# Kernel tuning notes

Hardware: AMD Instinct MI355X
Metric: run time of the kernel (lower is better)

Reference implementation:

```python
import jax, jax.numpy as jnp
import numpy as np

N, E, D = 100000, 1600000, 128      # nodes, edges, in_channels = MLP out_dim
L = 3                               # num GIN layers
OC = D + L * D                      # concat width = 512
CH, CHID = 4, 256                   # num ChannelMLPs, their hidden dim


def setup_inputs() -> dict:
    key = jax.random.key(0)
    ks = jax.random.split(key, 10)
    s = lambda fan_in: 1.0 / np.sqrt(fan_in)
    x = jax.random.normal(ks[0], (N, D), dtype=jnp.float32)
    edge_index = jax.random.randint(ks[1], (2, E), 0, N, dtype=jnp.int32)
    # conv MLPs: per layer 3 linear layers (in->hid, hid->hid, hid->out), all 128x128
    convW = jax.random.normal(ks[2], (L, 3, D, D), dtype=jnp.float32) * s(D)
    convB = jnp.zeros((L, 3, D), dtype=jnp.float32)
    # channel MLPs: 512 -> 256 -> 256 -> 1, ReLU after every layer (output_activation='relu')
    chanW1 = jax.random.normal(ks[3], (CH, OC, CHID), dtype=jnp.float32) * s(OC)
    chanB1 = jnp.zeros((CH, CHID), dtype=jnp.float32)
    chanW2 = jax.random.normal(ks[4], (CH, CHID, CHID), dtype=jnp.float32) * s(CHID)
    chanB2 = jnp.zeros((CH, CHID), dtype=jnp.float32)
    chanW3 = jax.random.normal(ks[5], (CH, CHID, 1), dtype=jnp.float32) * s(CHID)
    chanB3 = jnp.zeros((CH, 1), dtype=jnp.float32)
    return {"x": x, "edge_index": edge_index, "convW": convW, "convB": convB,
            "chanW1": chanW1, "chanB1": chanB1, "chanW2": chanW2, "chanB2": chanB2,
            "chanW3": chanW3, "chanB3": chanB3}


def reference(x, edge_index, convW, convB, chanW1, chanB1, chanW2, chanB2, chanW3, chanB3):
    src, dst = edge_index[0], edge_index[1]
    n = x.shape[0]
    feats = [x]                      # skip_first_features=False -> keep input
    h = x
    for l in range(L):
        # GINConv, eps=0: mlp((1+eps)*h + sum_{j in N(i)} h_j)
        agg = jax.ops.segment_sum(h[src], dst, num_segments=n)  # scatter-add at targets
        h = h + agg
        for k in range(3):           # MLP: Lin+ReLU x3 (2 hidden + relu output activation)
            h = jax.nn.relu(h @ convW[l, k] + convB[l, k])
        feats.append(h)
    xcat = jnp.concatenate(feats, axis=1)                       # [N, 512]
    # channel MLPs vectorized over the channel axis c
    h1 = jax.nn.relu(jnp.einsum('nd,cdh->cnh', xcat, chanW1) + chanB1[:, None, :])
    h2 = jax.nn.relu(jnp.einsum('cnh,chk->cnk', h1, chanW2) + chanB2[:, None, :])
    h3 = jax.nn.relu(jnp.einsum('cnh,cho->cno', h2, chanW3) + chanB3[:, None, :])
    return jnp.transpose(h3[..., 0])                            # [N, num_ChannelMLPs]
```

## Files before the change

kernel.cpp:

```cpp
#include <hip/hip_runtime.h>
#include <hip/hip_bf16.h>

#define D 128
#define NLAYER 3
#define NCH 4

typedef __attribute__((ext_vector_type(8))) short short8;
typedef __attribute__((ext_vector_type(4))) float f32x4;

__device__ __forceinline__ ushort f2bf(float f) {
    unsigned int u = __builtin_bit_cast(unsigned int, f);
    u += 0x7fffu + ((u >> 16) & 1u);
    return (ushort)(u >> 16);
}
__device__ __forceinline__ float bflo(unsigned int u) {
    return __builtin_bit_cast(float, u << 16);
}
__device__ __forceinline__ float bfhi(unsigned int u) {
    return __builtin_bit_cast(float, u & 0xffff0000u);
}

#define FILL_CHUNK 4096
__global__ __launch_bounds__(256) void hist_part_kernel(
    const int* __restrict__ dst, int* __restrict__ deg,
    int E, int nPer, int N)
{
    int cls = blockIdx.x & 7;
    int base = (blockIdx.x >> 3) * FILL_CHUNK;
    int lo = cls * nPer;
    int hi = lo + nPer; if (hi > N) hi = N;
    int end = base + FILL_CHUNK; if (end > E) end = E;
    for (int e = base + threadIdx.x; e < end; e += 256) {
        int d = dst[e];
        if (d >= lo && d < hi) atomicAdd(&deg[d], 1);
    }
}

__global__ __launch_bounds__(256) void blocksum_kernel(
    const int* __restrict__ deg, int* __restrict__ bsum, int n)
{
    int i = blockIdx.x * 256 + threadIdx.x;
    int v = (i < n) ? deg[i] : 0;
#pragma unroll
    for (int o = 1; o < 64; o <<= 1) v += __shfl_xor(v, o);
    __shared__ int s[4];
    if ((threadIdx.x & 63) == 0) s[threadIdx.x >> 6] = v;
    __syncthreads();
    if (threadIdx.x == 0) bsum[blockIdx.x] = s[0] + s[1] + s[2] + s[3];
}

__global__ __launch_bounds__(512) void scanblk_kernel(
    const int* __restrict__ bsum, int* __restrict__ boff, int nb,
    int* __restrict__ offs, int n, int E)
{
    __shared__ int sh[512];
    int t = threadIdx.x;
    sh[t] = (t < nb) ? bsum[t] : 0;
    __syncthreads();
    for (int d = 1; d < 512; d <<= 1) {
        int v = (t >= d) ? sh[t - d] : 0;
        __syncthreads();
        sh[t] += v;
        __syncthreads();
    }
    if (t < nb) boff[t] = (t == 0) ? 0 : sh[t - 1];
    if (t == 0) offs[n] = E;
}

__global__ __launch_bounds__(256) void blockscan_kernel(
    const int* __restrict__ deg, const int* __restrict__ boff,
    int* __restrict__ offs, int* __restrict__ cursor, int n)
{
    __shared__ int sh[256];
    int t = threadIdx.x;
    int i = blockIdx.x * 256 + t;
    int v = (i < n) ? deg[i] : 0;
    sh[t] = v;
    __syncthreads();
    for (int d = 1; d < 256; d <<= 1) {
        int u = (t >= d) ? sh[t - d] : 0;
        __syncthreads();
        sh[t] += u;
        __syncthreads();
    }
    if (i < n) {
        int ex = boff[blockIdx.x] + sh[t] - v;
        offs[i] = ex; cursor[i] = ex;
    }
}

__global__ __launch_bounds__(256) void fill_part_kernel(
    const int* __restrict__ src, const int* __restrict__ dst,
    int* __restrict__ cursor, int* __restrict__ csr,
    int E, int nPer, int N)
{
    int cls = blockIdx.x & 7;
    int base = (blockIdx.x >> 3) * FILL_CHUNK;
    int lo = cls * nPer;
    int hi = lo + nPer; if (hi > N) hi = N;
    int end = base + FILL_CHUNK; if (end > E) end = E;
    for (int e = base + threadIdx.x; e < end; e += 256) {
        int d = dst[e];
        int s = src[e];
        if (d >= lo && d < hi) {
            int p = atomicAdd(&cursor[d], 1);
            csr[p] = s;
        }
    }
}

__global__ __launch_bounds__(256) void cvtx_kernel(
    const float* __restrict__ x, ushort* __restrict__ xb, int total8)
{
    int i = blockIdx.x * 256 + threadIdx.x;
    if (i >= total8) return;
    const float* gp = x + (size_t)i * 8;
    float4 v0 = *(const float4*)gp;
    float4 v1 = *(const float4*)(gp + 4);
    short8 pk;
    pk[0] = (short)f2bf(v0.x); pk[1] = (short)f2bf(v0.y);
    pk[2] = (short)f2bf(v0.z); pk[3] = (short)f2bf(v0.w);
    pk[4] = (short)f2bf(v1.x); pk[5] = (short)f2bf(v1.y);
    pk[6] = (short)f2bf(v1.z); pk[7] = (short)f2bf(v1.w);
    *(short8*)(xb + (size_t)i * 8) = pk;
}

__global__ void cvtW_kernel(const float* __restrict__ W, ushort* __restrict__ Wt,
                            int K, int Ncols) {
    __shared__ float tile[32][33];
    int c = blockIdx.z;
    int k0 = blockIdx.x * 32, n0 = blockIdx.y * 32;
    const float* Wc = W + (size_t)c * K * Ncols;
    ushort* Wtc = Wt + (size_t)c * K * Ncols;
    int tx = threadIdx.x & 31, ty = threadIdx.x >> 5;
#pragma unroll
    for (int i = 0; i < 4; ++i) {
        int k = k0 + ty + i * 8;
        tile[ty + i * 8][tx] = Wc[(size_t)k * Ncols + n0 + tx];
    }
    __syncthreads();
#pragma unroll
    for (int i = 0; i < 4; ++i) {
        int n = n0 + ty + i * 8;
        Wtc[(size_t)n * K + k0 + tx] = f2bf(tile[tx][ty + i * 8]);
    }
}

__global__ __launch_bounds__(256) void agg_bf16(
    const ushort* __restrict__ h,
    const int* __restrict__ offs, const int* __restrict__ csr,
    ushort* __restrict__ outb, int n)
{
    int node = (blockIdx.x * 256 + threadIdx.x) >> 4;
    int l16 = threadIdx.x & 15;
    if (node >= n) return;
    uint4 u = *((const uint4*)(h + (size_t)node * 128) + l16);
    float a0 = bflo(u.x), a1 = bfhi(u.x);
    float a2 = bflo(u.y), a3 = bfhi(u.y);
    float a4 = bflo(u.z), a5 = bfhi(u.z);
    float a6 = bflo(u.w), a7 = bfhi(u.w);
    int b = offs[node], e = offs[node + 1];
    int j = b;
    for (; j + 4 <= e; j += 4) {
        int s0 = csr[j], s1 = csr[j + 1], s2 = csr[j + 2], s3 = csr[j + 3];
        uint4 v0 = *((const uint4*)(h + (size_t)s0 * 128) + l16);
        uint4 v1 = *((const uint4*)(h + (size_t)s1 * 128) + l16);
        uint4 v2 = *((const uint4*)(h + (size_t)s2 * 128) + l16);
        uint4 v3 = *((const uint4*)(h + (size_t)s3 * 128) + l16);
        a0 += (bflo(v0.x) + bflo(v1.x)) + (bflo(v2.x) + bflo(v3.x));
        a1 += (bfhi(v0.x) + bfhi(v1.x)) + (bfhi(v2.x) + bfhi(v3.x));
        a2 += (bflo(v0.y) + bflo(v1.y)) + (bflo(v2.y) + bflo(v3.y));
        a3 += (bfhi(v0.y) + bfhi(v1.y)) + (bfhi(v2.y) + bfhi(v3.y));
        a4 += (bflo(v0.z) + bflo(v1.z)) + (bflo(v2.z) + bflo(v3.z));
        a5 += (bfhi(v0.z) + bfhi(v1.z)) + (bfhi(v2.z) + bfhi(v3.z));
        a6 += (bflo(v0.w) + bflo(v1.w)) + (bflo(v2.w) + bflo(v3.w));
        a7 += (bfhi(v0.w) + bfhi(v1.w)) + (bfhi(v2.w) + bfhi(v3.w));
    }
    for (; j < e; ++j) {
        uint4 v0 = *((const uint4*)(h + (size_t)csr[j] * 128) + l16);
        a0 += bflo(v0.x); a1 += bfhi(v0.x);
        a2 += bflo(v0.y); a3 += bfhi(v0.y);
        a4 += bflo(v0.z); a5 += bfhi(v0.z);
        a6 += bflo(v0.w); a7 += bfhi(v0.w);
    }
    uint4 po;
    po.x = (unsigned int)f2bf(a0) | ((unsigned int)f2bf(a1) << 16);
    po.y = (unsigned int)f2bf(a2) | ((unsigned int)f2bf(a3) << 16);
    po.z = (unsigned int)f2bf(a4) | ((unsigned int)f2bf(a5) << 16);
    po.w = (unsigned int)f2bf(a6) | ((unsigned int)f2bf(a7) << 16);
    *((uint4*)(outb + (size_t)node * 128) + l16) = po;
}

__global__ __launch_bounds__(256) void gin_mlp_mfma(
    const ushort* __restrict__ A,
    const ushort* __restrict__ WtL,
    const float* __restrict__ biasL,
    ushort* __restrict__ Out,
    int nrows)
{
    __shared__ __align__(16) ushort As[128 * 128];
    __shared__ __align__(16) ushort Bs[128 * 128];
    const int t = threadIdx.x;
    const int w = t >> 6, lane = t & 63;
    const int quad = lane >> 4, c15 = lane & 15;
    const int wr = w >> 1, wc = w & 1;
    const int rowbase = blockIdx.x * 128;

#pragma unroll
    for (int i = 0; i < 8; ++i) {
        int lin = (i * 4 + w) * 64 + lane;
        int row = lin >> 4, slot = lin & 15, g = slot ^ (row & 15);
        int grow = rowbase + row;
        if (grow >= nrows) grow = 0;
        const ushort* gp = A + (size_t)grow * 128 + g * 8;
        __builtin_amdgcn_global_load_lds(
            (const __attribute__((address_space(1))) void*)gp,
            (__attribute__((address_space(3))) void*)&As[(i * 4 + w) * 512],
            16, 0, 0);
    }
#pragma unroll
    for (int i = 0; i < 8; ++i) {
        int lin = (i * 4 + w) * 64 + lane;
        int n = lin >> 4, slot = lin & 15, g = slot ^ (n & 15);
        const ushort* gp = WtL + (size_t)n * 128 + g * 8;
        __builtin_amdgcn_global_load_lds(
            (const __attribute__((address_space(1))) void*)gp,
            (__attribute__((address_space(3))) void*)&Bs[(i * 4 + w) * 512],
            16, 0, 0);
    }
    __syncthreads();

    for (int s = 0; s < 3; ++s) {
        f32x4 acc[4][4];
#pragma unroll
        for (int i = 0; i < 4; ++i)
#pragma unroll
            for (int j = 0; j < 4; ++j)
#pragma unroll
                for (int r = 0; r < 4; ++r) acc[i][j][r] = 0.f;

#pragma unroll
        for (int ks = 0; ks < 4; ++ks) {
            short8 af[4], bf[4];
#pragma unroll
            for (int tr = 0; tr < 4; ++tr) {
                int r = wr * 64 + tr * 16 + c15;
                af[tr] = *(const short8*)&As[r * 128 + (((ks * 4 + quad) ^ (r & 15)) * 8)];
            }
#pragma unroll
            for (int tc = 0; tc < 4; ++tc) {
                int n = wc * 64 + tc * 16 + c15;
                bf[tc] = *(const short8*)&Bs[n * 128 + (((ks * 4 + quad) ^ (n & 15)) * 8)];
            }
#pragma unroll
            for (int tr = 0; tr < 4; ++tr)
#pragma unroll
                for (int tc = 0; tc < 4; ++tc)
                    acc[tr][tc] = __builtin_amdgcn_mfma_f32_16x16x32_bf16(
                        af[tr], bf[tc], acc[tr][tc], 0, 0, 0);
        }
        __syncthreads();

        if (s < 2) {
#pragma unroll
            for (int tc = 0; tc < 4; ++tc) {
                int col = wc * 64 + tc * 16 + c15;
                float bv = biasL[s * 128 + col];
#pragma unroll
                for (int tr = 0; tr < 4; ++tr)
#pragma unroll
                    for (int rg = 0; rg < 4; ++rg) {
                        int row = wr * 64 + tr * 16 + quad * 4 + rg;
                        As[row * 128 + (((col >> 3) ^ (row & 15)) * 8) + (col & 7)]
                            = f2bf(fmaxf(acc[tr][tc][rg] + bv, 0.f));
                    }
            }
            const ushort* Wn = WtL + (size_t)(s + 1) * 128 * 128;
#pragma unroll
            for (int i = 0; i < 8; ++i) {
                int lin = (i * 4 + w) * 64 + lane;
                int n = lin >> 4, slot = lin & 15, g = slot ^ (n & 15);
                const ushort* gp = Wn + (size_t)n * 128 + g * 8;
                __builtin_amdgcn_global_load_lds(
                    (const __attribute__((address_space(1))) void*)gp,
                    (__attribute__((address_space(3))) void*)&Bs[(i * 4 + w) * 512],
                    16, 0, 0);
            }
            __syncthreads();
        } else {
#pragma unroll
            for (int tc = 0; tc < 4; ++tc) {
                int col = wc * 64 + tc * 16 + c15;
                float bv = biasL[2 * 128 + col];
#pragma unroll
                for (int tr = 0; tr < 4; ++tr)
#pragma unroll
                    for (int rg = 0; rg < 4; ++rg) {
                        int grow = rowbase + wr * 64 + tr * 16 + quad * 4 + rg;
                        if (grow < nrows)
                            Out[(size_t)grow * 128 + col]
                                = f2bf(fmaxf(acc[tr][tc][rg] + bv, 0.f));
                    }
            }
        }
    }
}

__global__ __launch_bounds__(256, 2) void chan_fused_mfma(
    const ushort* __restrict__ A0, const ushort* __restrict__ A1,
    const ushort* __restrict__ A2, const ushort* __restrict__ A3,
    const ushort* __restrict__ Wt1,
    const float* __restrict__ b1,
    const ushort* __restrict__ Wt2,
    const float* __restrict__ b2,
    const float* __restrict__ w3,
    const float* __restrict__ b3,
    float* __restrict__ out,
    int N, int T, int chunkT)
{
    const int bid = blockIdx.x;
    const int xcd = bid & 7;
    const int idx = bid >> 3;
    const int c = idx & 3;
    const int rt = xcd * chunkT + (idx >> 2);
    if (rt >= T) return;
    const int rowbase = rt * 64;

    __shared__ __align__(16) ushort Bs2[2][256 * 64];
    __shared__ float red[64][4];
    ushort* Ts = &Bs2[1][0];

    const int t = threadIdx.x;
    const int w = t >> 6, lane = t & 63;
    const int quad = lane >> 4, c15 = lane & 15;
    const ushort* W1c = Wt1 + (size_t)c * 256 * 512;
    const ushort* W2c = Wt2 + (size_t)c * 256 * 256;

    int b_n[8], b_g[8];
#pragma unroll
    for (int i = 0; i < 8; ++i) {
        int lin = (i * 4 + w) * 64 + lane;
        b_n[i] = lin >> 3;
        b_g[i] = (lin & 7) ^ (b_n[i] & 7);
    }
    auto stageB = [&](int buf, const ushort* Wn, int ldk, int kc) {
#pragma unroll
        for (int i = 0; i < 8; ++i) {
            const ushort* gp = Wn + (size_t)b_n[i] * ldk + kc + b_g[i] * 8;
            __builtin_amdgcn_global_load_lds(
                (const __attribute__((address_space(1))) void*)gp,
                (__attribute__((address_space(3))) void*)&Bs2[buf][(i * 4 + w) * 512],
                16, 0, 0);
        }
    };

    int growv[4];
#pragma unroll
    for (int tr = 0; tr < 4; ++tr) {
        int g = rowbase + tr * 16 + c15;
        growv[tr] = (g < N) ? g : 0;
    }
    auto loadA = [&](short8 (&dst)[4][2], int kc) {
        int ai = kc >> 7;
        const ushort* Ab = (ai == 0) ? A0 : (ai == 1) ? A1 : (ai == 2) ? A2 : A3;
        const int within = kc & 127;
#pragma unroll
        for (int tr = 0; tr < 4; ++tr) {
            const ushort* rp = Ab + (size_t)growv[tr] * 128 + within + quad * 8;
            dst[tr][0] = *(const short8*)(rp);
            dst[tr][1] = *(const short8*)(rp + 32);
        }
    };

    f32x4 acc[4][4];
#pragma unroll
    for (int i = 0; i < 4; ++i)
#pragma unroll
        for (int j = 0; j < 4; ++j)
#pragma unroll
            for (int r = 0; r < 4; ++r) acc[i][j][r] = 0.f;

    short8 afb[2][4][2];
    loadA(afb[0], 0);
    stageB(0, W1c, 512, 0);
    __syncthreads();
#pragma unroll
    for (int s = 0; s < 8; ++s) {
        const int cur = s & 1, nxt = cur ^ 1;
        if (s < 7) {
            loadA(afb[nxt], (s + 1) * 64);
            stageB(nxt, W1c, 512, (s + 1) * 64);
        } else {
            stageB(0, W2c, 256, 0);
        }
#pragma unroll
        for (int ks = 0; ks < 2; ++ks) {
            short8 bf[4];
#pragma unroll
            for (int tc = 0; tc < 4; ++tc) {
                int n = w * 64 + tc * 16 + c15;
                bf[tc] = *(const short8*)&Bs2[cur][n * 64 + (((ks * 4 + quad) ^ (n & 7)) * 8)];
            }
#pragma unroll
            for (int tr = 0; tr < 4; ++tr)
#pragma unroll
                for (int tc = 0; tc < 4; ++tc)
                    acc[tr][tc] = __builtin_amdgcn_mfma_f32_16x16x32_bf16(
                        afb[cur][tr][ks], bf[tc], acc[tr][tc], 0, 0, 0);
        }
        __syncthreads();
    }

#pragma unroll
    for (int tc = 0; tc < 4; ++tc) {
        int col = w * 64 + tc * 16 + c15;
        float bv = b1[c * 256 + col];
#pragma unroll
        for (int tr = 0; tr < 4; ++tr)
#pragma unroll
            for (int rg = 0; rg < 4; ++rg) {
                int row = tr * 16 + quad * 4 + rg;
                Ts[row * 256 + (((col >> 3) ^ (row & 31)) * 8) + (col & 7)]
                    = f2bf(fmaxf(acc[tr][tc][rg] + bv, 0.f));
            }
    }
    __syncthreads();

#pragma unroll
    for (int i = 0; i < 4; ++i)
#pragma unroll
        for (int j = 0; j < 4; ++j)
#pragma unroll
            for (int r = 0; r < 4; ++r) acc[i][j][r] = 0.f;

#pragma unroll
    for (int s = 0; s < 4; ++s) {
#pragma unroll
        for (int ks = 0; ks < 2; ++ks) {
            short8 af[4], bf[4];
            const int g0 = s * 8 + ks * 4 + quad;
#pragma unroll
            for (int tr = 0; tr < 4; ++tr) {
                int r = tr * 16 + c15;
                af[tr] = *(const short8*)&Ts[r * 256 + ((g0 ^ (r & 31)) * 8)];
            }
#pragma unroll
            for (int tc = 0; tc < 4; ++tc) {
                int n = w * 64 + tc * 16 + c15;
                bf[tc] = *(const short8*)&Bs2[0][n * 64 + (((ks * 4 + quad) ^ (n & 7)) * 8)];
            }
#pragma unroll
            for (int tr = 0; tr < 4; ++tr)
#pragma unroll
                for (int tc = 0; tc < 4; ++tc)
                    acc[tr][tc] = __builtin_amdgcn_mfma_f32_16x16x32_bf16(
                        af[tr], bf[tc], acc[tr][tc], 0, 0, 0);
        }
        if (s < 3) {
            __syncthreads();
            stageB(0, W2c, 256, (s + 1) * 64);
            __syncthreads();
        }
    }

    float b2v[4], w3v[4];
#pragma unroll
    for (int tc = 0; tc < 4; ++tc) {
        int col = w * 64 + tc * 16 + c15;
        b2v[tc] = b2[c * 256 + col];
        w3v[tc] = w3[c * 256 + col];
    }
#pragma unroll
    for (int tr = 0; tr < 4; ++tr)
#pragma unroll
        for (int rg = 0; rg < 4; ++rg) {
            float p = 0.f;
#pragma unroll
            for (int tc = 0; tc < 4; ++tc)
                p += fmaxf(acc[tr][tc][rg] + b2v[tc], 0.f) * w3v[tc];
            p += __shfl_xor(p, 1);
            p += __shfl_xor(p, 2);
            p += __shfl_xor(p, 4);
            p += __shfl_xor(p, 8);
            if (c15 == 0) red[tr * 16 + quad * 4 + rg][w] = p;
        }
    __syncthreads();
    if (t < 64) {
        int grow = rowbase + t;
        if (grow < N) {
            float s = red[t][0] + red[t][1] + red[t][2] + red[t][3] + b3[c];
            out[(size_t)grow * NCH + c] = fmaxf(s, 0.f);
        }
    }
}

extern "C" void kernel_launch(void* const* d_in, const int* in_sizes, int n_in,
                              void* d_out, int out_size, void* d_ws, size_t ws_size,
                              hipStream_t stream) {
    const float* x        = (const float*)d_in[0];
    const int*   eidx     = (const int*)d_in[1];
    const float* convW    = (const float*)d_in[2];
    const float* convB    = (const float*)d_in[3];
    const float* chanW1   = (const float*)d_in[4];
    const float* chanB1   = (const float*)d_in[5];
    const float* chanW2   = (const float*)d_in[6];
    const float* chanB2   = (const float*)d_in[7];
    const float* chanW3   = (const float*)d_in[8];
    const float* chanB3   = (const float*)d_in[9];
    float* out = (float*)d_out;

    const int N = in_sizes[0] / D;
    const int E = in_sizes[1] / 2;
    const int* srcp = eidx;
    const int* dstp = eidx + E;
    const int nb = (N + 255) / 256;

    char* w = (char*)d_ws;
    auto take = [&](size_t bytes) {
        char* p = w;
        w += (bytes + 255) & ~(size_t)255;
        return p;
    };
    ushort* xb     = (ushort*)take((size_t)N * D * 2);
    ushort* h0     = (ushort*)take((size_t)N * D * 2);
    ushort* h1     = (ushort*)take((size_t)N * D * 2);
    ushort* h2     = (ushort*)take((size_t)N * D * 2);
    int*    deg    = (int*)take((size_t)N * 4);
    int*    offs   = (int*)take((size_t)(N + 1) * 4);
    int*    cursor = (int*)take((size_t)N * 4);
    int*    bsum   = (int*)take((size_t)nb * 4);
    int*    boff   = (int*)take((size_t)nb * 4);
    ushort* Wt1b   = (ushort*)take((size_t)NCH * 256 * 512 * 2);
    ushort* Wt2b   = (ushort*)take((size_t)NCH * 256 * 256 * 2);
    ushort* WtC    = (ushort*)take((size_t)NLAYER * 3 * D * D * 2);

    size_t used = (size_t)(w - (char*)d_ws);
    if (used > ws_size) return;
    size_t rem = ws_size - used;
    size_t need_gin = (((size_t)E * 4 + 255) & ~(size_t)255) + (size_t)N * D * 2;
    if (rem < need_gin) return;

    int*    csr = (int*)w;
    ushort* a   = (ushort*)(w + (((size_t)E * 4 + 255) & ~(size_t)255));

    hipMemsetAsync(deg, 0, (size_t)N * 4, stream);
    {
        int nchunks = (E + FILL_CHUNK - 1) / FILL_CHUNK;
        int nPer = (N + 7) / 8;
        hist_part_kernel<<<nchunks * 8, 256, 0, stream>>>(dstp, deg, E, nPer, N);
        blocksum_kernel<<<nb, 256, 0, stream>>>(deg, bsum, N);
        scanblk_kernel<<<1, 512, 0, stream>>>(bsum, boff, nb, offs, N, E);
        blockscan_kernel<<<nb, 256, 0, stream>>>(deg, boff, offs, cursor, N);
        fill_part_kernel<<<nchunks * 8, 256, 0, stream>>>(
            srcp, dstp, cursor, csr, E, nPer, N);
    }

    cvtx_kernel<<<(N * 16 + 255) / 256, 256, 0, stream>>>(x, xb, N * 16);
    cvtW_kernel<<<dim3(512 / 32, 256 / 32, NCH), 256, 0, stream>>>(chanW1, Wt1b, 512, 256);
    cvtW_kernel<<<dim3(256 / 32, 256 / 32, NCH), 256, 0, stream>>>(chanW2, Wt2b, 256, 256);
    cvtW_kernel<<<dim3(D / 32, D / 32, NLAYER * 3), 256, 0, stream>>>(convW, WtC, D, D);

    const int rowtiles = (N + 127) / 128;
    const int aggblocks = (N * 16 + 255) / 256;

    ushort* hbuf[NLAYER] = {h0, h1, h2};
    const ushort* prev = xb;
    for (int l = 0; l < NLAYER; ++l) {
        agg_bf16<<<aggblocks, 256, 0, stream>>>(prev, offs, csr, a, N);
        gin_mlp_mfma<<<rowtiles, 256, 0, stream>>>(
            a, WtC + (size_t)l * 3 * D * D, convB + (size_t)l * 3 * D, hbuf[l], N);
        prev = hbuf[l];
    }

    {
        const int T = (N + 63) / 64;
        const int chunkT = (T + 7) / 8;
        const int grid = 8 * chunkT * NCH;
        chan_fused_mfma<<<grid, 256, 0, stream>>>(
            xb, h0, h1, h2,
            Wt1b, chanB1, Wt2b, chanB2, chanW3, chanB3,
            out, N, T, chunkT);
    }
}
```

Before: 925.0 us.

## Stage A tiles through LDS with async loads and fine-grained vmcnt waits

The fused channel-MLP kernel now loads its A operand (concatenated features) into a double-buffered LDS tile with global_load_lds, where it previously used direct per-lane global loads into registers. The per-stage __syncthreads is replaced by explicit s_waitcnt vmcnt(10) plus raw s_barrier, so the next stage's loads can stay in flight while the current stage computes. Staging of W2 moves after the first GEMM loop. The aim is to cut register pressure and redundant global traffic for A, and to overlap memory with MFMA work. This costs extra LDS (the reduction buffer is aliased onto the A buffer) and relies on hand-counted outstanding-load numbers for correctness.

```diff
diff --git a/kernel.cpp b/kernel.cpp
--- a/kernel.cpp
+++ b/kernel.cpp
@@ -326,9 +326,10 @@
     if (rt >= T) return;
     const int rowbase = rt * 64;
 
+    __shared__ __align__(16) ushort As2[2][64 * 64];
     __shared__ __align__(16) ushort Bs2[2][256 * 64];
-    __shared__ float red[64][4];
     ushort* Ts = &Bs2[1][0];
+    float (*red)[4] = (float (*)[4]) & As2[0][0];
 
     const int t = threadIdx.x;
     const int w = t >> 6, lane = t & 63;
@@ -336,6 +337,28 @@
     const ushort* W1c = Wt1 + (size_t)c * 256 * 512;
     const ushort* W2c = Wt2 + (size_t)c * 256 * 256;
 
+    int a_grow[2], a_g[2];
+#pragma unroll
+    for (int i = 0; i < 2; ++i) {
+        int lin = (i * 4 + w) * 64 + lane;
+        int row = lin >> 3, slot = lin & 7;
+        a_g[i] = slot ^ (row & 7);
+        int g = rowbase + row;
+        a_grow[i] = (g < N) ? g : 0;
+    }
+    auto stageA = [&](int buf, int kc) {
+        int ai = kc >> 7;
+        const ushort* Ab = (ai == 0) ? A0 : (ai == 1) ? A1 : (ai == 2) ? A2 : A3;
+        const int within = kc & 127;
+#pragma unroll
+        for (int i = 0; i < 2; ++i) {
+            const ushort* gp = Ab + (size_t)a_grow[i] * 128 + within + a_g[i] * 8;
+            __builtin_amdgcn_global_load_lds(
+                (const __attribute__((address_space(1))) void*)gp,
+                (__attribute__((address_space(3))) void*)&As2[buf][(i * 4 + w) * 512],
+                16, 0, 0);
+        }
+    };
     int b_n[8], b_g[8];
 #pragma unroll
     for (int i = 0; i < 8; ++i) {
@@ -354,24 +377,6 @@
         }
     };
 
-    int growv[4];
-#pragma unroll
-    for (int tr = 0; tr < 4; ++tr) {
-        int g = rowbase + tr * 16 + c15;
-        growv[tr] = (g < N) ? g : 0;
-    }
-    auto loadA = [&](short8 (&dst)[4][2], int kc) {
-        int ai = kc >> 7;
-        const ushort* Ab = (ai == 0) ? A0 : (ai == 1) ? A1 : (ai == 2) ? A2 : A3;
-        const int within = kc & 127;
-#pragma unroll
-        for (int tr = 0; tr < 4; ++tr) {
-            const ushort* rp = Ab + (size_t)growv[tr] * 128 + within + quad * 8;
-            dst[tr][0] = *(const short8*)(rp);
-            dst[tr][1] = *(const short8*)(rp + 32);
-        }
-    };
-
     f32x4 acc[4][4];
 #pragma unroll
     for (int i = 0; i < 4; ++i)
@@ -380,22 +385,28 @@
 #pragma unroll
             for (int r = 0; r < 4; ++r) acc[i][j][r] = 0.f;
 
-    short8 afb[2][4][2];
-    loadA(afb[0], 0);
-    stageB(0, W1c, 512, 0);
-    __syncthreads();
+    stageA(1, 0);
+    stageB(1, W1c, 512, 0);
 #pragma unroll
     for (int s = 0; s < 8; ++s) {
-        const int cur = s & 1, nxt = cur ^ 1;
+        const int cur = (s + 1) & 1;
         if (s < 7) {
-            loadA(afb[nxt], (s + 1) * 64);
-            stageB(nxt, W1c, 512, (s + 1) * 64);
+            stageA(cur ^ 1, (s + 1) * 64);
+            stageB(cur ^ 1, W1c, 512, (s + 1) * 64);
+            asm volatile("s_waitcnt vmcnt(10)" ::: "memory");
         } else {
-            stageB(0, W2c, 256, 0);
-        }
+            asm volatile("s_waitcnt vmcnt(0)" ::: "memory");
+        }
+        __builtin_amdgcn_s_barrier();
+        __builtin_amdgcn_sched_barrier(0);
 #pragma unroll
         for (int ks = 0; ks < 2; ++ks) {
-            short8 bf[4];
+            short8 af[4], bf[4];
+#pragma unroll
+            for (int tr = 0; tr < 4; ++tr) {
+                int r = tr * 16 + c15;
+                af[tr] = *(const short8*)&As2[cur][r * 64 + (((ks * 4 + quad) ^ (r & 7)) * 8)];
+            }
 #pragma unroll
             for (int tc = 0; tc < 4; ++tc) {
                 int n = w * 64 + tc * 16 + c15;
@@ -406,11 +417,12 @@
 #pragma unroll
                 for (int tc = 0; tc < 4; ++tc)
                     acc[tr][tc] = __builtin_amdgcn_mfma_f32_16x16x32_bf16(
-                        afb[cur][tr][ks], bf[tc], acc[tr][tc], 0, 0, 0);
-        }
-        __syncthreads();
-    }
-
+                        af[tr], bf[tc], acc[tr][tc], 0, 0, 0);
+        }
+        __builtin_amdgcn_s_barrier();
+    }
+
+    stageB(0, W2c, 256, 0);
 #pragma unroll
     for (int tc = 0; tc < 4; ++tc) {
         int col = w * 64 + tc * 16 + c15;
@@ -470,6 +482,7 @@
         b2v[tc] = b2[c * 256 + col];
         w3v[tc] = w3[c * 256 + col];
     }
+    __syncthreads();
 #pragma unroll
     for (int tr = 0; tr < 4; ++tr)
 #pragma unroll
```

Result: faster. 822.2 us (-11.1%).
